# Optimization experiments

Measured on AMD Instinct MI355X. Metric: run time of the kernel, lower is better.

The kernel has to match this reference:

```python
import jax, jax.numpy as jnp
import numpy as np

NUM_HEADS = 16


def setup_inputs() -> dict:
    key = jax.random.key(0)
    ks = jax.random.split(key, 5)
    B, S, D = 4, 2048, 1024
    scale = 1.0 / np.sqrt(D)
    return {
        "x": jax.random.normal(ks[0], (B, S, D), dtype=jnp.float32),
        "q_proj": jax.random.normal(ks[1], (D, D), dtype=jnp.float32) * scale,
        "k_proj": jax.random.normal(ks[2], (D, D), dtype=jnp.float32) * scale,
        "v_proj": jax.random.normal(ks[3], (D, D), dtype=jnp.float32) * scale,
        "o_proj": jax.random.normal(ks[4], (D, D), dtype=jnp.float32) * scale,
    }


def reference(x, q_proj, k_proj, v_proj, o_proj):
    B, S, D = x.shape
    H = NUM_HEADS
    hd = D // H
    # projections: weight is [d_out, d_in]
    q = jnp.einsum('bsd,kd->bsk', x, q_proj)
    k = jnp.einsum('bsd,kd->bsk', x, k_proj)
    v = jnp.einsum('bsd,kd->bsk', x, v_proj)
    # split heads: [B, H, S, hd]
    q = q.reshape(B, S, H, hd).transpose(0, 2, 1, 3)
    k = k.reshape(B, S, H, hd).transpose(0, 2, 1, 3)
    v = v.reshape(B, S, H, hd).transpose(0, 2, 1, 3)
    scores = jnp.einsum('bhqd,bhkd->bhqk', q, k) / jnp.sqrt(jnp.asarray(hd, dtype=x.dtype))
    causal = jnp.tril(jnp.ones((S, S), dtype=bool))  # True = keep
    scores = jnp.where(causal, scores, -jnp.inf)
    attn = jax.nn.softmax(scores, axis=-1)
    out = jnp.einsum('bhqk,bhkd->bhqd', attn, v)
    out = out.transpose(0, 2, 1, 3).reshape(B, S, D)
    return jnp.einsum('bsv,mv->bsm', out, o_proj)
```

## Files before the change

kernel.cpp:

```cpp
#include <hip/hip_runtime.h>
#include <hip/hip_bf16.h>
#include <stdint.h>


typedef __bf16 bf16x8 __attribute__((ext_vector_type(8)));
typedef __bf16 bf16x4 __attribute__((ext_vector_type(4)));
typedef float  f32x4  __attribute__((ext_vector_type(4)));

static __device__ __forceinline__ f32x4 mfma16(bf16x8 a, bf16x8 b, f32x4 c) {
  return __builtin_amdgcn_mfma_f32_16x16x32_bf16(a, b, c, 0, 0, 0);
}

static __device__ __forceinline__ void load16_lds(const void* g, void* l) {
  __builtin_amdgcn_global_load_lds(
      (const __attribute__((address_space(1))) unsigned int*)g,
      (__attribute__((address_space(3))) unsigned int*)l, 16, 0, 0);
}

__global__ __launch_bounds__(256) void cvt_all(
    const float* __restrict__ x,
    const float* __restrict__ w0, const float* __restrict__ w1,
    const float* __restrict__ w2, const float* __restrict__ w3,
    __bf16* __restrict__ xb, __bf16* __restrict__ wqk,
    __bf16* __restrict__ wvb, __bf16* __restrict__ wob) {
  const int blk = blockIdx.x;
  const int t = threadIdx.x;
  if (blk < 4096) {
    int i = blk * 256 + t;
    const float4* in4 = (const float4*)x;
    float4 a = in4[2 * i], b = in4[2 * i + 1];
    __bf16 v[8];
    v[0] = (__bf16)a.x; v[1] = (__bf16)a.y; v[2] = (__bf16)a.z; v[3] = (__bf16)a.w;
    v[4] = (__bf16)b.x; v[5] = (__bf16)b.y; v[6] = (__bf16)b.z; v[7] = (__bf16)b.w;
    *(bf16x8*)(xb + 8 * i) = *(bf16x8*)v;
  } else {
    int b2 = blk - 4096;
    int m = b2 >> 9;
    const float* src = (m == 0) ? w0 : (m == 1) ? w1 : (m == 2) ? w2 : w3;
    __bf16* dst = (m == 0) ? wqk : (m == 1) ? (wqk + (size_t)(1024 * 1024))
                : (m == 2) ? wvb : wob;
    const float scl = (m == 0) ? 0.18033688011112042f : 1.0f;
    int i = (b2 & 511) * 256 + t;
    const float4* in4 = (const float4*)src;
    float4 a = in4[2 * i], b = in4[2 * i + 1];
    __bf16 v[8];
    v[0] = (__bf16)(a.x * scl); v[1] = (__bf16)(a.y * scl);
    v[2] = (__bf16)(a.z * scl); v[3] = (__bf16)(a.w * scl);
    v[4] = (__bf16)(b.x * scl); v[5] = (__bf16)(b.y * scl);
    v[6] = (__bf16)(b.z * scl); v[7] = (__bf16)(b.w * scl);
    *(bf16x8*)(dst + 8 * i) = *(bf16x8*)v;
  }
}

static __device__ __forceinline__ void stage_unit(
    const __bf16* __restrict__ X, long grow0, int K, long k0,
    __bf16* lds, int t) {
  const int lane = t & 63, w = t >> 6;
  const int rl = w * 8 + (lane >> 3);
  const int chunk = (lane & 7) ^ ((lane >> 3) & 7);
  load16_lds(X + (grow0 + rl) * (long)K + k0 + chunk * 8,
             lds + (w * 8) * 64);
}

template <typename OutT>
__global__ __launch_bounds__(512, 2) void gemm_bt8(
    const __bf16* __restrict__ A, const __bf16* __restrict__ Bw,
    OutT* __restrict__ C, int M, int N, int K, int NX) {
  __shared__ __align__(16) __bf16 As[3][256 * 64];
  __shared__ __align__(16) __bf16 Bs[3][128 * 64];
  const int t = threadIdx.x;
  const int lane = t & 63, w = t >> 6;
  const int wm = w >> 1, wn = w & 1;
  const int l15 = lane & 15, quad = lane >> 4;

  const int bid = blockIdx.x;
  const int cpx = gridDim.x >> 3;
  const int swz = (bid & 7) * cpx + (bid >> 3);
  const long m0 = (long)(swz / NX) * 256;
  const long n0 = (long)(swz % NX) * 128;

  int aoff[4][2], boff[4][2];
#pragma unroll
  for (int mf = 0; mf < 4; mf++)
#pragma unroll
    for (int ks = 0; ks < 2; ks++)
      aoff[mf][ks] = (wm * 64 + mf * 16 + l15) * 64 + (((ks * 4 + quad) ^ (l15 & 7)) << 3);
#pragma unroll
  for (int nf = 0; nf < 4; nf++)
#pragma unroll
    for (int ks = 0; ks < 2; ks++)
      boff[nf][ks] = (wn * 64 + nf * 16 + l15) * 64 + (((ks * 4 + quad) ^ (l15 & 7)) << 3);

  const int NT = K >> 6;
  __bf16 *Ac = As[0], *An = As[1], *Asg = As[2];
  __bf16 *Bc = Bs[0], *Bn = Bs[1], *Bsg = Bs[2];

#pragma unroll
  for (int u = 0; u < 4; u++) stage_unit(A, m0 + u * 64, K, 0, Ac + u * 64 * 64, t);
#pragma unroll
  for (int u = 0; u < 2; u++) stage_unit(Bw, n0 + u * 64, K, 0, Bc + u * 64 * 64, t);
#pragma unroll
  for (int u = 0; u < 4; u++) stage_unit(A, m0 + u * 64, K, 64, An + u * 64 * 64, t);
#pragma unroll
  for (int u = 0; u < 2; u++) stage_unit(Bw, n0 + u * 64, K, 64, Bn + u * 64 * 64, t);
  asm volatile("s_waitcnt vmcnt(6)" ::: "memory");
  __builtin_amdgcn_s_barrier();

  f32x4 acc[4][4] = {};
  for (int T = 0; T < NT; T++) {
    const bool pf2 = (T + 2 < NT);
    const long kn2 = (long)(T + 2) * 64;

    bf16x8 bfr[4][2];
#pragma unroll
    for (int nf = 0; nf < 4; nf++)
#pragma unroll
      for (int ks = 0; ks < 2; ks++)
        bfr[nf][ks] = *(const bf16x8*)(Bc + boff[nf][ks]);
    {
      bf16x8 a00 = *(const bf16x8*)(Ac + aoff[0][0]);
      bf16x8 a01 = *(const bf16x8*)(Ac + aoff[0][1]);
      bf16x8 a10 = *(const bf16x8*)(Ac + aoff[1][0]);
      bf16x8 a11 = *(const bf16x8*)(Ac + aoff[1][1]);
      if (pf2) {
#pragma unroll
        for (int u = 0; u < 4; u++)
          stage_unit(A, m0 + u * 64, K, kn2, Asg + u * 64 * 64, t);
      }
      __builtin_amdgcn_s_barrier();
      asm volatile("s_waitcnt lgkmcnt(0)" ::: "memory");
      __builtin_amdgcn_sched_barrier(0);
      __builtin_amdgcn_s_setprio(1);
#pragma unroll
      for (int nf = 0; nf < 4; nf++) {
        acc[0][nf] = mfma16(a00, bfr[nf][0], acc[0][nf]);
        acc[0][nf] = mfma16(a01, bfr[nf][1], acc[0][nf]);
        acc[1][nf] = mfma16(a10, bfr[nf][0], acc[1][nf]);
        acc[1][nf] = mfma16(a11, bfr[nf][1], acc[1][nf]);
      }
      __builtin_amdgcn_s_setprio(0);
      __builtin_amdgcn_s_barrier();
    }
    {
      bf16x8 a00 = *(const bf16x8*)(Ac + aoff[2][0]);
      bf16x8 a01 = *(const bf16x8*)(Ac + aoff[2][1]);
      bf16x8 a10 = *(const bf16x8*)(Ac + aoff[3][0]);
      bf16x8 a11 = *(const bf16x8*)(Ac + aoff[3][1]);
      if (pf2) {
#pragma unroll
        for (int u = 0; u < 2; u++)
          stage_unit(Bw, n0 + u * 64, K, kn2, Bsg + u * 64 * 64, t);
        asm volatile("s_waitcnt vmcnt(6)" ::: "memory");
      } else {
        asm volatile("s_waitcnt vmcnt(0)" ::: "memory");
      }
      __builtin_amdgcn_s_barrier();
      asm volatile("s_waitcnt lgkmcnt(0)" ::: "memory");
      __builtin_amdgcn_sched_barrier(0);
      __builtin_amdgcn_s_setprio(1);
#pragma unroll
      for (int nf = 0; nf < 4; nf++) {
        acc[2][nf] = mfma16(a00, bfr[nf][0], acc[2][nf]);
        acc[2][nf] = mfma16(a01, bfr[nf][1], acc[2][nf]);
        acc[3][nf] = mfma16(a10, bfr[nf][0], acc[3][nf]);
        acc[3][nf] = mfma16(a11, bfr[nf][1], acc[3][nf]);
      }
      __builtin_amdgcn_s_setprio(0);
      __builtin_amdgcn_s_barrier();
    }
    __bf16* ta = Ac; Ac = An; An = Asg; Asg = ta;
    __bf16* tb = Bc; Bc = Bn; Bn = Bsg; Bsg = tb;
  }

#pragma unroll
  for (int mf = 0; mf < 4; mf++)
#pragma unroll
    for (int nf = 0; nf < 4; nf++)
#pragma unroll
      for (int r = 0; r < 4; r++) {
        long row = m0 + wm * 64 + mf * 16 + quad * 4 + r;
        long col = n0 + wn * 64 + nf * 16 + l15;
        float v = acc[mf][nf][r];
        if constexpr (sizeof(OutT) == 2) C[row * (long)N + col] = (OutT)(__bf16)v;
        else                             C[row * (long)N + col] = v;
      }
}

__global__ __launch_bounds__(256) void attn4(
    const __bf16* __restrict__ QK, const __bf16* __restrict__ VT,
    __bf16* __restrict__ O) {
  constexpr int SD = 2048;
  constexpr int LDP = 72;
  __shared__ __align__(16) __bf16 Ks[3][64 * 64];
  __shared__ __align__(16) __bf16 Vs[3][64 * 64];
  __shared__ __align__(16) __bf16 Pw[4 * 32 * LDP];
  const int t = threadIdx.x;
  const int lane = t & 63, w = t >> 6;
  const int l15 = lane & 15, quad = lane >> 4;

  const int bid = blockIdx.x;
  const int g = (bid & 7) * 8 + (bid >> 6);
  const int jj = (bid >> 3) & 7;
  const int h = g & 15, b = g >> 4;

  const long qbase = (long)b * 2048 * SD + h * 64;
  const long kbase = qbase + 1024;
  __bf16* Pme = Pw + w * 32 * LDP;

  const int sr = w * 16 + (lane >> 3);
  const int scg = (lane & 7) ^ (sr & 7);
  const int ldsOff = (w * 16) * 64;
  const __bf16* gK = QK + kbase + (long)sr * SD + scg * 8;
  const __bf16* gV = VT + (long)(h * 64 + sr) * 8192 + b * 2048 + scg * 8;

  int kvoff[4][2];
#pragma unroll
  for (int nt = 0; nt < 4; nt++)
#pragma unroll
    for (int kk = 0; kk < 2; kk++)
      kvoff[nt][kk] = (nt * 16 + l15) * 64 + (((kk * 4 + quad) ^ (l15 & 7)) << 3);

  bf16x8 ones;
#pragma unroll
  for (int j = 0; j < 8; j++) ones[j] = (__bf16)1.0f;

#pragma unroll
  for (int half = 0; half < 2; half++) {
    const int qt = half ? (15 - jj) : jj;
    const int q0 = qt * 128;
    const int wrow0 = q0 + w * 32;

    bf16x8 qf[2][2];
#pragma unroll
    for (int mt = 0; mt < 2; mt++)
#pragma unroll
      for (int kk = 0; kk < 2; kk++)
        qf[mt][kk] = *(const bf16x8*)(QK + qbase +
            (long)(wrow0 + mt * 16 + l15) * SD + kk * 32 + quad * 8);

    f32x4 o_acc[2][4] = {};
    f32x4 o_l[2] = {};

    const int nkt = 2 * qt + 2;

    __syncthreads();
    load16_lds(gK, Ks[0] + ldsOff);
    load16_lds(gK + 8 * SD, Ks[0] + ldsOff + 8 * 64);
    load16_lds(gV, Vs[0] + ldsOff);
    load16_lds(gV + 8 * 8192, Vs[0] + ldsOff + 8 * 64);
    {
      const __bf16* gK1 = gK + (long)64 * SD;
      const __bf16* gV1 = gV + 64;
      load16_lds(gK1, Ks[1] + ldsOff);
      load16_lds(gK1 + 8 * SD, Ks[1] + ldsOff + 8 * 64);
      load16_lds(gV1, Vs[1] + ldsOff);
      load16_lds(gV1 + 8 * 8192, Vs[1] + ldsOff + 8 * 64);
    }

    int cur = 0;
    for (int kt = 0; kt < nkt; kt++) {
      if (kt + 1 < nkt) asm volatile("s_waitcnt vmcnt(4)" ::: "memory");
      else              asm volatile("s_waitcnt vmcnt(0)" ::: "memory");
      __builtin_amdgcn_s_barrier();
      __builtin_amdgcn_sched_barrier(0);

      if (kt + 2 < nkt) {
        int stg = cur + 2; if (stg >= 3) stg -= 3;
        const __bf16* gKn = gK + (long)(kt + 2) * 64 * SD;
        const __bf16* gVn = gV + (kt + 2) * 64;
        load16_lds(gKn, Ks[stg] + ldsOff);
        load16_lds(gKn + 8 * SD, Ks[stg] + ldsOff + 8 * 64);
        load16_lds(gVn, Vs[stg] + ldsOff);
        load16_lds(gVn + 8 * 8192, Vs[stg] + ldsOff + 8 * 64);
      }

      const int k0 = kt * 64;
      if (k0 <= wrow0 + 31) {
        const __bf16* KsB = Ks[cur];
        const __bf16* VsB = Vs[cur];
        bf16x8 kf[4][2];
#pragma unroll
        for (int nt = 0; nt < 4; nt++)
#pragma unroll
          for (int kk = 0; kk < 2; kk++)
            kf[nt][kk] = *(const bf16x8*)(KsB + kvoff[nt][kk]);
        f32x4 st[4][2];
        __builtin_amdgcn_s_setprio(1);
#pragma unroll
        for (int nt = 0; nt < 4; nt++)
#pragma unroll
          for (int mt = 0; mt < 2; mt++) {
            f32x4 z = {0.f, 0.f, 0.f, 0.f};
            z = mfma16(kf[nt][0], qf[mt][0], z);
            st[nt][mt] = mfma16(kf[nt][1], qf[mt][1], z);
          }
        __builtin_amdgcn_s_setprio(0);

        if (k0 + 63 <= wrow0) {
#pragma unroll
          for (int mt = 0; mt < 2; mt++)
#pragma unroll
            for (int nt = 0; nt < 4; nt++) {
              bf16x4 pb;
#pragma unroll
              for (int r = 0; r < 4; r++)
                pb[r] = (__bf16)__builtin_amdgcn_exp2f(st[nt][mt][r]);
              *(bf16x4*)(Pme + (mt * 16 + l15) * LDP + nt * 16 + quad * 4) = pb;
            }
        } else {
#pragma unroll
          for (int mt = 0; mt < 2; mt++) {
            const int qrow = wrow0 + mt * 16 + l15;
#pragma unroll
            for (int nt = 0; nt < 4; nt++) {
              const int keyb = k0 + nt * 16 + quad * 4;
              bf16x4 pb;
#pragma unroll
              for (int r = 0; r < 4; r++) {
                float e = __builtin_amdgcn_exp2f(st[nt][mt][r]);
                if (keyb + r > qrow) e = 0.f;
                pb[r] = (__bf16)e;
              }
              *(bf16x4*)(Pme + (mt * 16 + l15) * LDP + nt * 16 + quad * 4) = pb;
            }
          }
        }

#pragma unroll
        for (int kk = 0; kk < 2; kk++) {
          bf16x8 vf[4];
#pragma unroll
          for (int dt = 0; dt < 4; dt++)
            vf[dt] = *(const bf16x8*)(VsB + kvoff[dt][kk]);
#pragma unroll
          for (int mt = 0; mt < 2; mt++) {
            bf16x8 pf = *(const bf16x8*)(Pme + (mt * 16 + l15) * LDP + kk * 32 + quad * 8);
            __builtin_amdgcn_s_setprio(1);
#pragma unroll
            for (int dt = 0; dt < 4; dt++)
              o_acc[mt][dt] = mfma16(pf, vf[dt], o_acc[mt][dt]);
            o_l[mt] = mfma16(pf, ones, o_l[mt]);
            __builtin_amdgcn_s_setprio(0);
          }
        }
      }
      cur = (cur == 2) ? 0 : cur + 1;
    }

#pragma unroll
    for (int mt = 0; mt < 2; mt++) {
#pragma unroll
      for (int r = 0; r < 4; r++) {
        float inv = 1.f / o_l[mt][r];
        int row = wrow0 + mt * 16 + quad * 4 + r;
        long ob = ((long)b * 2048 + row) * 1024 + h * 64;
#pragma unroll
        for (int dt = 0; dt < 4; dt++)
          O[ob + dt * 16 + l15] = (__bf16)(o_acc[mt][dt][r] * inv);
      }
    }
  }
}

extern "C" void kernel_launch(void* const* d_in, const int* in_sizes, int n_in,
                              void* d_out, int out_size, void* d_ws, size_t ws_size,
                              hipStream_t stream) {
  const float* x  = (const float*)d_in[0];
  const float* wq = (const float*)d_in[1];
  const float* wk = (const float*)d_in[2];
  const float* wv = (const float*)d_in[3];
  const float* wo = (const float*)d_in[4];
  float* out = (float*)d_out;

  char* ws = (char*)d_ws;
  __bf16* xb   = (__bf16*)(ws);
  __bf16* wqk  = (__bf16*)(ws + (16l << 20));
  __bf16* wvb  = (__bf16*)(ws + (20l << 20));
  __bf16* wob  = (__bf16*)(ws + (22l << 20));
  __bf16* QK   = (__bf16*)(ws + (24l << 20));
  __bf16* VTg  = (__bf16*)(ws + (56l << 20));
  __bf16* Ab   = xb;

  cvt_all<<<6144, 256, 0, stream>>>(x, wq, wk, wv, wo, xb, wqk, wvb, wob);

  gemm_bt8<__bf16><<<512, 512, 0, stream>>>(xb, wqk, QK, 8192, 2048, 1024, 16);

  gemm_bt8<__bf16><<<256, 512, 0, stream>>>(wvb, xb, VTg, 1024, 8192, 1024, 64);

  attn4<<<512, 256, 0, stream>>>(QK, VTg, Ab);

  gemm_bt8<float><<<256, 512, 0, stream>>>(Ab, wob, out, 8192, 1024, 1024, 8);
}
```

Before: 229.5 us.

## Launch one query tile per block and switch attention to double-buffered K/V

The attention kernel previously had each block process two query tiles, paired for causal load balance (jj and 15-jj). Now it launches 1024 blocks, each handling one query tile, and orders tiles heaviest-first so the scheduler can balance the work. The K/V LDS pipeline also shrinks from three stages to two with a full vmcnt(0) wait each iteration. This lowers LDS use, which may allow more resident blocks, but exposes more load latency per iteration.

```diff
diff --git a/kernel.cpp b/kernel.cpp
--- a/kernel.cpp
+++ b/kernel.cpp
@@ -186,21 +186,21 @@
       }
 }
 
-__global__ __launch_bounds__(256) void attn4(
+__global__ __launch_bounds__(256) void attn5(
     const __bf16* __restrict__ QK, const __bf16* __restrict__ VT,
     __bf16* __restrict__ O) {
   constexpr int SD = 2048;
   constexpr int LDP = 72;
-  __shared__ __align__(16) __bf16 Ks[3][64 * 64];
-  __shared__ __align__(16) __bf16 Vs[3][64 * 64];
+  __shared__ __align__(16) __bf16 Ks[2][64 * 64];
+  __shared__ __align__(16) __bf16 Vs[2][64 * 64];
   __shared__ __align__(16) __bf16 Pw[4 * 32 * LDP];
   const int t = threadIdx.x;
   const int lane = t & 63, w = t >> 6;
   const int l15 = lane & 15, quad = lane >> 4;
 
   const int bid = blockIdx.x;
-  const int g = (bid & 7) * 8 + (bid >> 6);
-  const int jj = (bid >> 3) & 7;
+  const int g = (bid & 7) * 8 + (bid >> 7);
+  const int qt = 15 - ((bid >> 3) & 15);
   const int h = g & 15, b = g >> 4;
 
   const long qbase = (long)b * 2048 * SD + h * 64;
@@ -224,140 +224,125 @@
 #pragma unroll
   for (int j = 0; j < 8; j++) ones[j] = (__bf16)1.0f;
 
-#pragma unroll
-  for (int half = 0; half < 2; half++) {
-    const int qt = half ? (15 - jj) : jj;
-    const int q0 = qt * 128;
-    const int wrow0 = q0 + w * 32;
-
-    bf16x8 qf[2][2];
-#pragma unroll
-    for (int mt = 0; mt < 2; mt++)
-#pragma unroll
-      for (int kk = 0; kk < 2; kk++)
-        qf[mt][kk] = *(const bf16x8*)(QK + qbase +
-            (long)(wrow0 + mt * 16 + l15) * SD + kk * 32 + quad * 8);
-
-    f32x4 o_acc[2][4] = {};
-    f32x4 o_l[2] = {};
-
-    const int nkt = 2 * qt + 2;
-
-    __syncthreads();
-    load16_lds(gK, Ks[0] + ldsOff);
-    load16_lds(gK + 8 * SD, Ks[0] + ldsOff + 8 * 64);
-    load16_lds(gV, Vs[0] + ldsOff);
-    load16_lds(gV + 8 * 8192, Vs[0] + ldsOff + 8 * 64);
-    {
-      const __bf16* gK1 = gK + (long)64 * SD;
-      const __bf16* gV1 = gV + 64;
-      load16_lds(gK1, Ks[1] + ldsOff);
-      load16_lds(gK1 + 8 * SD, Ks[1] + ldsOff + 8 * 64);
-      load16_lds(gV1, Vs[1] + ldsOff);
-      load16_lds(gV1 + 8 * 8192, Vs[1] + ldsOff + 8 * 64);
-    }
-
-    int cur = 0;
-    for (int kt = 0; kt < nkt; kt++) {
-      if (kt + 1 < nkt) asm volatile("s_waitcnt vmcnt(4)" ::: "memory");
-      else              asm volatile("s_waitcnt vmcnt(0)" ::: "memory");
-      __builtin_amdgcn_s_barrier();
-      __builtin_amdgcn_sched_barrier(0);
-
-      if (kt + 2 < nkt) {
-        int stg = cur + 2; if (stg >= 3) stg -= 3;
-        const __bf16* gKn = gK + (long)(kt + 2) * 64 * SD;
-        const __bf16* gVn = gV + (kt + 2) * 64;
-        load16_lds(gKn, Ks[stg] + ldsOff);
-        load16_lds(gKn + 8 * SD, Ks[stg] + ldsOff + 8 * 64);
-        load16_lds(gVn, Vs[stg] + ldsOff);
-        load16_lds(gVn + 8 * 8192, Vs[stg] + ldsOff + 8 * 64);
-      }
-
-      const int k0 = kt * 64;
-      if (k0 <= wrow0 + 31) {
-        const __bf16* KsB = Ks[cur];
-        const __bf16* VsB = Vs[cur];
-        bf16x8 kf[4][2];
-#pragma unroll
-        for (int nt = 0; nt < 4; nt++)
-#pragma unroll
-          for (int kk = 0; kk < 2; kk++)
-            kf[nt][kk] = *(const bf16x8*)(KsB + kvoff[nt][kk]);
-        f32x4 st[4][2];
-        __builtin_amdgcn_s_setprio(1);
-#pragma unroll
-        for (int nt = 0; nt < 4; nt++)
-#pragma unroll
-          for (int mt = 0; mt < 2; mt++) {
-            f32x4 z = {0.f, 0.f, 0.f, 0.f};
-            z = mfma16(kf[nt][0], qf[mt][0], z);
-            st[nt][mt] = mfma16(kf[nt][1], qf[mt][1], z);
+  const int q0 = qt * 128;
+  const int wrow0 = q0 + w * 32;
+
+  bf16x8 qf[2][2];
+#pragma unroll
+  for (int mt = 0; mt < 2; mt++)
+#pragma unroll
+    for (int kk = 0; kk < 2; kk++)
+      qf[mt][kk] = *(const bf16x8*)(QK + qbase +
+          (long)(wrow0 + mt * 16 + l15) * SD + kk * 32 + quad * 8);
+
+  f32x4 o_acc[2][4] = {};
+  f32x4 o_l[2] = {};
+
+  const int nkt = 2 * qt + 2;
+
+  load16_lds(gK, Ks[0] + ldsOff);
+  load16_lds(gK + 8 * SD, Ks[0] + ldsOff + 8 * 64);
+  load16_lds(gV, Vs[0] + ldsOff);
+  load16_lds(gV + 8 * 8192, Vs[0] + ldsOff + 8 * 64);
+
+  int cur = 0;
+  for (int kt = 0; kt < nkt; kt++) {
+    asm volatile("s_waitcnt vmcnt(0) lgkmcnt(0)" ::: "memory");
+    __builtin_amdgcn_s_barrier();
+    __builtin_amdgcn_sched_barrier(0);
+
+    if (kt + 1 < nkt) {
+      const __bf16* gKn = gK + (long)(kt + 1) * 64 * SD;
+      const __bf16* gVn = gV + (kt + 1) * 64;
+      load16_lds(gKn, Ks[cur ^ 1] + ldsOff);
+      load16_lds(gKn + 8 * SD, Ks[cur ^ 1] + ldsOff + 8 * 64);
+      load16_lds(gVn, Vs[cur ^ 1] + ldsOff);
+      load16_lds(gVn + 8 * 8192, Vs[cur ^ 1] + ldsOff + 8 * 64);
+    }
+
+    const int k0 = kt * 64;
+    if (k0 <= wrow0 + 31) {
+      const __bf16* KsB = Ks[cur];
+      const __bf16* VsB = Vs[cur];
+      bf16x8 kf[4][2];
+#pragma unroll
+      for (int nt = 0; nt < 4; nt++)
+#pragma unroll
+        for (int kk = 0; kk < 2; kk++)
+          kf[nt][kk] = *(const bf16x8*)(KsB + kvoff[nt][kk]);
+      f32x4 st[4][2];
+      __builtin_amdgcn_s_setprio(1);
+#pragma unroll
+      for (int nt = 0; nt < 4; nt++)
+#pragma unroll
+        for (int mt = 0; mt < 2; mt++) {
+          f32x4 z = {0.f, 0.f, 0.f, 0.f};
+          z = mfma16(kf[nt][0], qf[mt][0], z);
+          st[nt][mt] = mfma16(kf[nt][1], qf[mt][1], z);
+        }
+      __builtin_amdgcn_s_setprio(0);
+
+      if (k0 + 63 <= wrow0) {
+#pragma unroll
+        for (int mt = 0; mt < 2; mt++)
+#pragma unroll
+          for (int nt = 0; nt < 4; nt++) {
+            bf16x4 pb;
+#pragma unroll
+            for (int r = 0; r < 4; r++)
+              pb[r] = (__bf16)__builtin_amdgcn_exp2f(st[nt][mt][r]);
+            *(bf16x4*)(Pme + (mt * 16 + l15) * LDP + nt * 16 + quad * 4) = pb;
           }
-        __builtin_amdgcn_s_setprio(0);
-
-        if (k0 + 63 <= wrow0) {
-#pragma unroll
-          for (int mt = 0; mt < 2; mt++)
-#pragma unroll
-            for (int nt = 0; nt < 4; nt++) {
-              bf16x4 pb;
-#pragma unroll
-              for (int r = 0; r < 4; r++)
-                pb[r] = (__bf16)__builtin_amdgcn_exp2f(st[nt][mt][r]);
-              *(bf16x4*)(Pme + (mt * 16 + l15) * LDP + nt * 16 + quad * 4) = pb;
+      } else {
+#pragma unroll
+        for (int mt = 0; mt < 2; mt++) {
+          const int qrow = wrow0 + mt * 16 + l15;
+#pragma unroll
+          for (int nt = 0; nt < 4; nt++) {
+            const int keyb = k0 + nt * 16 + quad * 4;
+            bf16x4 pb;
+#pragma unroll
+            for (int r = 0; r < 4; r++) {
+              float e = __builtin_amdgcn_exp2f(st[nt][mt][r]);
+              if (keyb + r > qrow) e = 0.f;
+              pb[r] = (__bf16)e;
             }
-        } else {
-#pragma unroll
-          for (int mt = 0; mt < 2; mt++) {
-            const int qrow = wrow0 + mt * 16 + l15;
-#pragma unroll
-            for (int nt = 0; nt < 4; nt++) {
-              const int keyb = k0 + nt * 16 + quad * 4;
-              bf16x4 pb;
-#pragma unroll
-              for (int r = 0; r < 4; r++) {
-                float e = __builtin_amdgcn_exp2f(st[nt][mt][r]);
-                if (keyb + r > qrow) e = 0.f;
-                pb[r] = (__bf16)e;
-              }
-              *(bf16x4*)(Pme + (mt * 16 + l15) * LDP + nt * 16 + quad * 4) = pb;
-            }
+            *(bf16x4*)(Pme + (mt * 16 + l15) * LDP + nt * 16 + quad * 4) = pb;
           }
         }
-
-#pragma unroll
-        for (int kk = 0; kk < 2; kk++) {
-          bf16x8 vf[4];
+      }
+
+#pragma unroll
+      for (int kk = 0; kk < 2; kk++) {
+        bf16x8 vf[4];
+#pragma unroll
+        for (int dt = 0; dt < 4; dt++)
+          vf[dt] = *(const bf16x8*)(VsB + kvoff[dt][kk]);
+#pragma unroll
+        for (int mt = 0; mt < 2; mt++) {
+          bf16x8 pf = *(const bf16x8*)(Pme + (mt * 16 + l15) * LDP + kk * 32 + quad * 8);
+          __builtin_amdgcn_s_setprio(1);
 #pragma unroll
           for (int dt = 0; dt < 4; dt++)
-            vf[dt] = *(const bf16x8*)(VsB + kvoff[dt][kk]);
-#pragma unroll
-          for (int mt = 0; mt < 2; mt++) {
-            bf16x8 pf = *(const bf16x8*)(Pme + (mt * 16 + l15) * LDP + kk * 32 + quad * 8);
-            __builtin_amdgcn_s_setprio(1);
-#pragma unroll
-            for (int dt = 0; dt < 4; dt++)
-              o_acc[mt][dt] = mfma16(pf, vf[dt], o_acc[mt][dt]);
-            o_l[mt] = mfma16(pf, ones, o_l[mt]);
-            __builtin_amdgcn_s_setprio(0);
-          }
+            o_acc[mt][dt] = mfma16(pf, vf[dt], o_acc[mt][dt]);
+          o_l[mt] = mfma16(pf, ones, o_l[mt]);
+          __builtin_amdgcn_s_setprio(0);
         }
       }
-      cur = (cur == 2) ? 0 : cur + 1;
-    }
-
-#pragma unroll
-    for (int mt = 0; mt < 2; mt++) {
-#pragma unroll
-      for (int r = 0; r < 4; r++) {
-        float inv = 1.f / o_l[mt][r];
-        int row = wrow0 + mt * 16 + quad * 4 + r;
-        long ob = ((long)b * 2048 + row) * 1024 + h * 64;
-#pragma unroll
-        for (int dt = 0; dt < 4; dt++)
-          O[ob + dt * 16 + l15] = (__bf16)(o_acc[mt][dt][r] * inv);
-      }
+    }
+    cur ^= 1;
+  }
+
+#pragma unroll
+  for (int mt = 0; mt < 2; mt++) {
+#pragma unroll
+    for (int r = 0; r < 4; r++) {
+      float inv = 1.f / o_l[mt][r];
+      int row = wrow0 + mt * 16 + quad * 4 + r;
+      long ob = ((long)b * 2048 + row) * 1024 + h * 64;
+#pragma unroll
+      for (int dt = 0; dt < 4; dt++)
+        O[ob + dt * 16 + l15] = (__bf16)(o_acc[mt][dt][r] * inv);
     }
   }
 }
@@ -387,7 +372,7 @@
 
   gemm_bt8<__bf16><<<256, 512, 0, stream>>>(wvb, xb, VTg, 1024, 8192, 1024, 64);
 
-  attn4<<<512, 256, 0, stream>>>(QK, VTg, Ab);
+  attn5<<<1024, 256, 0, stream>>>(QK, VTg, Ab);
 
   gemm_bt8<float><<<256, 512, 0, stream>>>(Ab, wob, out, 8192, 1024, 1024, 8);
 }
```

Result: slower. 250.4 us (+9.1%).

## Enlarge attention query tile to 256 rows with 8 waves per block

Applied to the files above, without the earlier changes.

The attention kernel now uses 512 threads (8 waves) per block, each block handling 256 query rows per half instead of 128. Every K/V tile staged in shared memory therefore serves twice as many query rows, which halves global K/V traffic per query, and each thread issues one async load per tile instead of two. The grid shrinks from 512 to 256 blocks, which reduces parallelism and may give a coarser causal load balance. The larger P scratch buffer also raises shared memory use, which can limit occupancy.

```diff
diff --git a/kernel.cpp b/kernel.cpp
--- a/kernel.cpp
+++ b/kernel.cpp
@@ -186,30 +186,30 @@
       }
 }
 
-__global__ __launch_bounds__(256) void attn4(
+__global__ __launch_bounds__(512, 2) void attn6(
     const __bf16* __restrict__ QK, const __bf16* __restrict__ VT,
     __bf16* __restrict__ O) {
   constexpr int SD = 2048;
   constexpr int LDP = 72;
   __shared__ __align__(16) __bf16 Ks[3][64 * 64];
   __shared__ __align__(16) __bf16 Vs[3][64 * 64];
-  __shared__ __align__(16) __bf16 Pw[4 * 32 * LDP];
+  __shared__ __align__(16) __bf16 Pw[8 * 32 * LDP];
   const int t = threadIdx.x;
   const int lane = t & 63, w = t >> 6;
   const int l15 = lane & 15, quad = lane >> 4;
 
   const int bid = blockIdx.x;
-  const int g = (bid & 7) * 8 + (bid >> 6);
-  const int jj = (bid >> 3) & 7;
+  const int g = (bid & 7) * 8 + (bid >> 5);
+  const int jj = (bid >> 3) & 3;
   const int h = g & 15, b = g >> 4;
 
   const long qbase = (long)b * 2048 * SD + h * 64;
   const long kbase = qbase + 1024;
   __bf16* Pme = Pw + w * 32 * LDP;
 
-  const int sr = w * 16 + (lane >> 3);
-  const int scg = (lane & 7) ^ (sr & 7);
-  const int ldsOff = (w * 16) * 64;
+  const int sr = t >> 3;
+  const int scg = (t & 7) ^ (sr & 7);
+  const int ldsOff = (w * 8) * 64;
   const __bf16* gK = QK + kbase + (long)sr * SD + scg * 8;
   const __bf16* gV = VT + (long)(h * 64 + sr) * 8192 + b * 2048 + scg * 8;
 
@@ -226,8 +226,8 @@
 
 #pragma unroll
   for (int half = 0; half < 2; half++) {
-    const int qt = half ? (15 - jj) : jj;
-    const int q0 = qt * 128;
+    const int qb = half ? (7 - jj) : jj;
+    const int q0 = qb * 256;
     const int wrow0 = q0 + w * 32;
 
     bf16x8 qf[2][2];
@@ -241,37 +241,25 @@
     f32x4 o_acc[2][4] = {};
     f32x4 o_l[2] = {};
 
-    const int nkt = 2 * qt + 2;
+    const int nkt = 4 * qb + 4;
 
     __syncthreads();
     load16_lds(gK, Ks[0] + ldsOff);
-    load16_lds(gK + 8 * SD, Ks[0] + ldsOff + 8 * 64);
     load16_lds(gV, Vs[0] + ldsOff);
-    load16_lds(gV + 8 * 8192, Vs[0] + ldsOff + 8 * 64);
-    {
-      const __bf16* gK1 = gK + (long)64 * SD;
-      const __bf16* gV1 = gV + 64;
-      load16_lds(gK1, Ks[1] + ldsOff);
-      load16_lds(gK1 + 8 * SD, Ks[1] + ldsOff + 8 * 64);
-      load16_lds(gV1, Vs[1] + ldsOff);
-      load16_lds(gV1 + 8 * 8192, Vs[1] + ldsOff + 8 * 64);
-    }
+    load16_lds(gK + (long)64 * SD, Ks[1] + ldsOff);
+    load16_lds(gV + 64, Vs[1] + ldsOff);
 
     int cur = 0;
     for (int kt = 0; kt < nkt; kt++) {
-      if (kt + 1 < nkt) asm volatile("s_waitcnt vmcnt(4)" ::: "memory");
+      if (kt + 1 < nkt) asm volatile("s_waitcnt vmcnt(2)" ::: "memory");
       else              asm volatile("s_waitcnt vmcnt(0)" ::: "memory");
       __builtin_amdgcn_s_barrier();
       __builtin_amdgcn_sched_barrier(0);
 
       if (kt + 2 < nkt) {
         int stg = cur + 2; if (stg >= 3) stg -= 3;
-        const __bf16* gKn = gK + (long)(kt + 2) * 64 * SD;
-        const __bf16* gVn = gV + (kt + 2) * 64;
-        load16_lds(gKn, Ks[stg] + ldsOff);
-        load16_lds(gKn + 8 * SD, Ks[stg] + ldsOff + 8 * 64);
-        load16_lds(gVn, Vs[stg] + ldsOff);
-        load16_lds(gVn + 8 * 8192, Vs[stg] + ldsOff + 8 * 64);
+        load16_lds(gK + (long)(kt + 2) * 64 * SD, Ks[stg] + ldsOff);
+        load16_lds(gV + (kt + 2) * 64, Vs[stg] + ldsOff);
       }
 
       const int k0 = kt * 64;
@@ -387,7 +375,7 @@
 
   gemm_bt8<__bf16><<<256, 512, 0, stream>>>(wvb, xb, VTg, 1024, 8192, 1024, 64);
 
-  attn4<<<512, 256, 0, stream>>>(QK, VTg, Ab);
+  attn6<<<256, 512, 0, stream>>>(QK, VTg, Ab);
 
   gemm_bt8<float><<<256, 512, 0, stream>>>(Ab, wob, out, 8192, 1024, 1024, 8);
 }
```

After: 231.1 us. Within noise of the previous version (+0.7%).

## Merge QK and V projection GEMMs into one launch; enlarge attention query tile

Applied to the files above, without the earlier changes.

The QK and transposed-V projection GEMMs now run as a single 768-block launch that dispatches each block to one of the two problems, which removes one kernel launch and the tail idle time between them. The attention kernel is reworked so each block handles one 256-row query tile with 64 rows per wave, instead of two 128-row tiles (a light one paired with a heavy one). This reuses each K/V tile loaded into LDS across more query rows and skips fully masked 16-row subtiles. In exchange it uses more accumulator registers per wave, and because causal work now differs between blocks, load balance depends on the block ordering.

```diff
diff --git a/kernel.cpp b/kernel.cpp
--- a/kernel.cpp
+++ b/kernel.cpp
@@ -63,21 +63,14 @@
 }
 
 template <typename OutT>
-__global__ __launch_bounds__(512, 2) void gemm_bt8(
+static __device__ __forceinline__ void gemm_core(
     const __bf16* __restrict__ A, const __bf16* __restrict__ Bw,
-    OutT* __restrict__ C, int M, int N, int K, int NX) {
+    OutT* __restrict__ C, int N, int K, long m0, long n0, int t) {
   __shared__ __align__(16) __bf16 As[3][256 * 64];
   __shared__ __align__(16) __bf16 Bs[3][128 * 64];
-  const int t = threadIdx.x;
   const int lane = t & 63, w = t >> 6;
   const int wm = w >> 1, wn = w & 1;
   const int l15 = lane & 15, quad = lane >> 4;
-
-  const int bid = blockIdx.x;
-  const int cpx = gridDim.x >> 3;
-  const int swz = (bid & 7) * cpx + (bid >> 3);
-  const long m0 = (long)(swz / NX) * 256;
-  const long n0 = (long)(swz % NX) * 128;
 
   int aoff[4][2], boff[4][2];
 #pragma unroll
@@ -186,26 +179,53 @@
       }
 }
 
-__global__ __launch_bounds__(256) void attn4(
+__global__ __launch_bounds__(512, 2) void gemm_dual(
+    const __bf16* __restrict__ xb, const __bf16* __restrict__ wqk,
+    const __bf16* __restrict__ wvb,
+    __bf16* __restrict__ QK, __bf16* __restrict__ VTg) {
+  const int bid = blockIdx.x;
+  const int swz = (bid & 7) * 96 + (bid >> 3);
+  if (swz < 512) {
+    gemm_core<__bf16>(xb, wqk, QK, 2048, 1024,
+                      (long)(swz / 16) * 256, (long)(swz % 16) * 128, threadIdx.x);
+  } else {
+    const int s = swz - 512;
+    gemm_core<__bf16>(wvb, xb, VTg, 8192, 1024,
+                      (long)(s / 64) * 256, (long)(s % 64) * 128, threadIdx.x);
+  }
+}
+
+__global__ __launch_bounds__(512, 2) void gemm_bt8(
+    const __bf16* __restrict__ A, const __bf16* __restrict__ Bw,
+    float* __restrict__ C, int M, int N, int K, int NX) {
+  const int bid = blockIdx.x;
+  const int cpx = gridDim.x >> 3;
+  const int swz = (bid & 7) * cpx + (bid >> 3);
+  gemm_core<float>(A, Bw, C, N, K, (long)(swz / NX) * 256, (long)(swz % NX) * 128,
+                   threadIdx.x);
+}
+
+__global__ __launch_bounds__(256) void attn7(
     const __bf16* __restrict__ QK, const __bf16* __restrict__ VT,
     __bf16* __restrict__ O) {
   constexpr int SD = 2048;
   constexpr int LDP = 72;
   __shared__ __align__(16) __bf16 Ks[3][64 * 64];
   __shared__ __align__(16) __bf16 Vs[3][64 * 64];
-  __shared__ __align__(16) __bf16 Pw[4 * 32 * LDP];
+  __shared__ __align__(16) __bf16 Pw[4 * 16 * LDP];
   const int t = threadIdx.x;
   const int lane = t & 63, w = t >> 6;
   const int l15 = lane & 15, quad = lane >> 4;
 
   const int bid = blockIdx.x;
-  const int g = (bid & 7) * 8 + (bid >> 6);
-  const int jj = (bid >> 3) & 7;
+  const int a = bid & 7, m3 = (bid >> 3) & 7, c = (bid >> 6) & 3, hi = bid >> 8;
+  const int g = a * 8 + c * 2 + hi;
+  const int qb = hi ? (7 - m3) : m3;
   const int h = g & 15, b = g >> 4;
 
   const long qbase = (long)b * 2048 * SD + h * 64;
   const long kbase = qbase + 1024;
-  __bf16* Pme = Pw + w * 32 * LDP;
+  __bf16* Pme = Pw + w * 16 * LDP;
 
   const int sr = w * 16 + (lane >> 3);
   const int scg = (lane & 7) ^ (sr & 7);
@@ -224,140 +244,130 @@
 #pragma unroll
   for (int j = 0; j < 8; j++) ones[j] = (__bf16)1.0f;
 
-#pragma unroll
-  for (int half = 0; half < 2; half++) {
-    const int qt = half ? (15 - jj) : jj;
-    const int q0 = qt * 128;
-    const int wrow0 = q0 + w * 32;
-
-    bf16x8 qf[2][2];
-#pragma unroll
-    for (int mt = 0; mt < 2; mt++)
-#pragma unroll
-      for (int kk = 0; kk < 2; kk++)
-        qf[mt][kk] = *(const bf16x8*)(QK + qbase +
-            (long)(wrow0 + mt * 16 + l15) * SD + kk * 32 + quad * 8);
-
-    f32x4 o_acc[2][4] = {};
-    f32x4 o_l[2] = {};
-
-    const int nkt = 2 * qt + 2;
-
-    __syncthreads();
-    load16_lds(gK, Ks[0] + ldsOff);
-    load16_lds(gK + 8 * SD, Ks[0] + ldsOff + 8 * 64);
-    load16_lds(gV, Vs[0] + ldsOff);
-    load16_lds(gV + 8 * 8192, Vs[0] + ldsOff + 8 * 64);
-    {
-      const __bf16* gK1 = gK + (long)64 * SD;
-      const __bf16* gV1 = gV + 64;
-      load16_lds(gK1, Ks[1] + ldsOff);
-      load16_lds(gK1 + 8 * SD, Ks[1] + ldsOff + 8 * 64);
-      load16_lds(gV1, Vs[1] + ldsOff);
-      load16_lds(gV1 + 8 * 8192, Vs[1] + ldsOff + 8 * 64);
+  const int q0 = qb * 256;
+  const int wrow0 = q0 + w * 64;
+
+  bf16x8 qf[4][2];
+#pragma unroll
+  for (int mt = 0; mt < 4; mt++)
+#pragma unroll
+    for (int kk = 0; kk < 2; kk++)
+      qf[mt][kk] = *(const bf16x8*)(QK + qbase +
+          (long)(wrow0 + mt * 16 + l15) * SD + kk * 32 + quad * 8);
+
+  f32x4 o_acc[4][4] = {};
+  f32x4 o_l[4] = {};
+
+  const int nkt = 4 * qb + 4;
+
+  load16_lds(gK, Ks[0] + ldsOff);
+  load16_lds(gK + 8 * SD, Ks[0] + ldsOff + 8 * 64);
+  load16_lds(gV, Vs[0] + ldsOff);
+  load16_lds(gV + 8 * 8192, Vs[0] + ldsOff + 8 * 64);
+  {
+    const __bf16* gK1 = gK + (long)64 * SD;
+    const __bf16* gV1 = gV + 64;
+    load16_lds(gK1, Ks[1] + ldsOff);
+    load16_lds(gK1 + 8 * SD, Ks[1] + ldsOff + 8 * 64);
+    load16_lds(gV1, Vs[1] + ldsOff);
+    load16_lds(gV1 + 8 * 8192, Vs[1] + ldsOff + 8 * 64);
+  }
+
+  int cur = 0;
+  for (int kt = 0; kt < nkt; kt++) {
+    if (kt + 1 < nkt) asm volatile("s_waitcnt vmcnt(4)" ::: "memory");
+    else              asm volatile("s_waitcnt vmcnt(0)" ::: "memory");
+    __builtin_amdgcn_s_barrier();
+    __builtin_amdgcn_sched_barrier(0);
+
+    if (kt + 2 < nkt) {
+      int stg = cur + 2; if (stg >= 3) stg -= 3;
+      const __bf16* gKn = gK + (long)(kt + 2) * 64 * SD;
+      const __bf16* gVn = gV + (kt + 2) * 64;
+      load16_lds(gKn, Ks[stg] + ldsOff);
+      load16_lds(gKn + 8 * SD, Ks[stg] + ldsOff + 8 * 64);
+      load16_lds(gVn, Vs[stg] + ldsOff);
+      load16_lds(gVn + 8 * 8192, Vs[stg] + ldsOff + 8 * 64);
     }
 
-    int cur = 0;
-    for (int kt = 0; kt < nkt; kt++) {
-      if (kt + 1 < nkt) asm volatile("s_waitcnt vmcnt(4)" ::: "memory");
-      else              asm volatile("s_waitcnt vmcnt(0)" ::: "memory");
-      __builtin_amdgcn_s_barrier();
-      __builtin_amdgcn_sched_barrier(0);
-
-      if (kt + 2 < nkt) {
-        int stg = cur + 2; if (stg >= 3) stg -= 3;
-        const __bf16* gKn = gK + (long)(kt + 2) * 64 * SD;
-        const __bf16* gVn = gV + (kt + 2) * 64;
-        load16_lds(gKn, Ks[stg] + ldsOff);
-        load16_lds(gKn + 8 * SD, Ks[stg] + ldsOff + 8 * 64);
-        load16_lds(gVn, Vs[stg] + ldsOff);
-        load16_lds(gVn + 8 * 8192, Vs[stg] + ldsOff + 8 * 64);
-      }
-
-      const int k0 = kt * 64;
-      if (k0 <= wrow0 + 31) {
-        const __bf16* KsB = Ks[cur];
-        const __bf16* VsB = Vs[cur];
-        bf16x8 kf[4][2];
-#pragma unroll
-        for (int nt = 0; nt < 4; nt++)
-#pragma unroll
-          for (int kk = 0; kk < 2; kk++)
-            kf[nt][kk] = *(const bf16x8*)(KsB + kvoff[nt][kk]);
-        f32x4 st[4][2];
+    const int k0 = kt * 64;
+    if (k0 <= wrow0 + 63) {
+      const __bf16* KsB = Ks[cur];
+      const __bf16* VsB = Vs[cur];
+      bf16x8 kf[4][2], vf[4][2];
+#pragma unroll
+      for (int nt = 0; nt < 4; nt++)
+#pragma unroll
+        for (int kk = 0; kk < 2; kk++) {
+          kf[nt][kk] = *(const bf16x8*)(KsB + kvoff[nt][kk]);
+          vf[nt][kk] = *(const bf16x8*)(VsB + kvoff[nt][kk]);
+        }
+
+#pragma unroll
+      for (int mt = 0; mt < 4; mt++) {
+        const int qlo = wrow0 + mt * 16;
+        if (k0 > qlo + 15) continue;
+
+        f32x4 st[4];
         __builtin_amdgcn_s_setprio(1);
 #pragma unroll
-        for (int nt = 0; nt < 4; nt++)
-#pragma unroll
-          for (int mt = 0; mt < 2; mt++) {
-            f32x4 z = {0.f, 0.f, 0.f, 0.f};
-            z = mfma16(kf[nt][0], qf[mt][0], z);
-            st[nt][mt] = mfma16(kf[nt][1], qf[mt][1], z);
+        for (int nt = 0; nt < 4; nt++) {
+          f32x4 z = {0.f, 0.f, 0.f, 0.f};
+          z = mfma16(kf[nt][0], qf[mt][0], z);
+          st[nt] = mfma16(kf[nt][1], qf[mt][1], z);
+        }
+        __builtin_amdgcn_s_setprio(0);
+
+        if (k0 + 63 <= qlo) {
+#pragma unroll
+          for (int nt = 0; nt < 4; nt++) {
+            bf16x4 pb;
+#pragma unroll
+            for (int r = 0; r < 4; r++)
+              pb[r] = (__bf16)__builtin_amdgcn_exp2f(st[nt][r]);
+            *(bf16x4*)(Pme + l15 * LDP + nt * 16 + quad * 4) = pb;
           }
-        __builtin_amdgcn_s_setprio(0);
-
-        if (k0 + 63 <= wrow0) {
-#pragma unroll
-          for (int mt = 0; mt < 2; mt++)
-#pragma unroll
-            for (int nt = 0; nt < 4; nt++) {
-              bf16x4 pb;
-#pragma unroll
-              for (int r = 0; r < 4; r++)
-                pb[r] = (__bf16)__builtin_amdgcn_exp2f(st[nt][mt][r]);
-              *(bf16x4*)(Pme + (mt * 16 + l15) * LDP + nt * 16 + quad * 4) = pb;
+        } else {
+          const int qrow = qlo + l15;
+#pragma unroll
+          for (int nt = 0; nt < 4; nt++) {
+            const int keyb = k0 + nt * 16 + quad * 4;
+            bf16x4 pb;
+#pragma unroll
+            for (int r = 0; r < 4; r++) {
+              float e = __builtin_amdgcn_exp2f(st[nt][r]);
+              if (keyb + r > qrow) e = 0.f;
+              pb[r] = (__bf16)e;
             }
-        } else {
-#pragma unroll
-          for (int mt = 0; mt < 2; mt++) {
-            const int qrow = wrow0 + mt * 16 + l15;
-#pragma unroll
-            for (int nt = 0; nt < 4; nt++) {
-              const int keyb = k0 + nt * 16 + quad * 4;
-              bf16x4 pb;
-#pragma unroll
-              for (int r = 0; r < 4; r++) {
-                float e = __builtin_amdgcn_exp2f(st[nt][mt][r]);
-                if (keyb + r > qrow) e = 0.f;
-                pb[r] = (__bf16)e;
-              }
-              *(bf16x4*)(Pme + (mt * 16 + l15) * LDP + nt * 16 + quad * 4) = pb;
-            }
+            *(bf16x4*)(Pme + l15 * LDP + nt * 16 + quad * 4) = pb;
           }
         }
 
 #pragma unroll
         for (int kk = 0; kk < 2; kk++) {
-          bf16x8 vf[4];
+          bf16x8 pf = *(const bf16x8*)(Pme + l15 * LDP + kk * 32 + quad * 8);
+          __builtin_amdgcn_s_setprio(1);
 #pragma unroll
           for (int dt = 0; dt < 4; dt++)
-            vf[dt] = *(const bf16x8*)(VsB + kvoff[dt][kk]);
-#pragma unroll
-          for (int mt = 0; mt < 2; mt++) {
-            bf16x8 pf = *(const bf16x8*)(Pme + (mt * 16 + l15) * LDP + kk * 32 + quad * 8);
-            __builtin_amdgcn_s_setprio(1);
-#pragma unroll
-            for (int dt = 0; dt < 4; dt++)
-              o_acc[mt][dt] = mfma16(pf, vf[dt], o_acc[mt][dt]);
-            o_l[mt] = mfma16(pf, ones, o_l[mt]);
-            __builtin_amdgcn_s_setprio(0);
-          }
+            o_acc[mt][dt] = mfma16(pf, vf[dt][kk], o_acc[mt][dt]);
+          o_l[mt] = mfma16(pf, ones, o_l[mt]);
+          __builtin_amdgcn_s_setprio(0);
         }
       }
-      cur = (cur == 2) ? 0 : cur + 1;
     }
-
-#pragma unroll
-    for (int mt = 0; mt < 2; mt++) {
-#pragma unroll
-      for (int r = 0; r < 4; r++) {
-        float inv = 1.f / o_l[mt][r];
-        int row = wrow0 + mt * 16 + quad * 4 + r;
-        long ob = ((long)b * 2048 + row) * 1024 + h * 64;
-#pragma unroll
-        for (int dt = 0; dt < 4; dt++)
-          O[ob + dt * 16 + l15] = (__bf16)(o_acc[mt][dt][r] * inv);
-      }
+    cur = (cur == 2) ? 0 : cur + 1;
+  }
+
+#pragma unroll
+  for (int mt = 0; mt < 4; mt++) {
+#pragma unroll
+    for (int r = 0; r < 4; r++) {
+      float inv = 1.f / o_l[mt][r];
+      int row = wrow0 + mt * 16 + quad * 4 + r;
+      long ob = ((long)b * 2048 + row) * 1024 + h * 64;
+#pragma unroll
+      for (int dt = 0; dt < 4; dt++)
+        O[ob + dt * 16 + l15] = (__bf16)(o_acc[mt][dt][r] * inv);
     }
   }
 }
@@ -383,11 +393,9 @@
 
   cvt_all<<<6144, 256, 0, stream>>>(x, wq, wk, wv, wo, xb, wqk, wvb, wob);
 
-  gemm_bt8<__bf16><<<512, 512, 0, stream>>>(xb, wqk, QK, 8192, 2048, 1024, 16);
-
-  gemm_bt8<__bf16><<<256, 512, 0, stream>>>(wvb, xb, VTg, 1024, 8192, 1024, 64);
-
-  attn4<<<512, 256, 0, stream>>>(QK, VTg, Ab);
-
-  gemm_bt8<float><<<256, 512, 0, stream>>>(Ab, wob, out, 8192, 1024, 1024, 8);
-}
+  gemm_dual<<<768, 512, 0, stream>>>(xb, wqk, wvb, QK, VTg);
+
+  attn7<<<512, 256, 0, stream>>>(QK, VTg, Ab);
+
+  gemm_bt8<<<256, 512, 0, stream>>>(Ab, wob, out, 8192, 1024, 1024, 8);
+}
```

Result: slower. 304.5 us (+32.7%).
